# Kernel tuning notes

Hardware: AMD Instinct MI355X
Metric: run time of the kernel (lower is better)

Reference implementation:

```python
import jax, jax.numpy as jnp
import numpy as np

B = 512          # graphs
NODES = 90       # nodes per graph (fixed by lin1 = Linear(90*L*H, ...))
N = B * NODES    # total nodes
F_IN = 90        # dataset.num_features
H = 128          # hidden
L = 3            # num_layers
HL = 64          # hidden_linear
C = 2            # dataset.num_classes
DEG = 16         # avg degree
E = N * DEG      # total edges


def setup_inputs() -> dict:
    key = jax.random.key(0)
    ks = jax.random.split(key, 14)
    x = jax.random.normal(ks[0], (N, F_IN), jnp.float32)
    # intra-graph random edges: graph g owns nodes [g*90, (g+1)*90)
    g = jnp.repeat(jnp.arange(B), NODES * DEG)
    src = g * NODES + jax.random.randint(ks[1], (E,), 0, NODES)
    dst = g * NODES + jax.random.randint(ks[2], (E,), 0, NODES)
    edge_index = jnp.stack([src, dst]).astype(jnp.int64)
    edge_attr = jax.random.uniform(ks[3], (E,), jnp.float32, 0.1, 1.0)
    batch = jnp.repeat(jnp.arange(B), NODES).astype(jnp.int64)

    def lin(k, fi, fo):
        s = 1.0 / np.sqrt(fi)
        kw, kb = jax.random.split(k)
        return (jax.random.uniform(kw, (fi, fo), jnp.float32, -s, s),
                jax.random.uniform(kb, (fo,), jnp.float32, -s, s))

    W1, b1 = lin(ks[4], F_IN, H)
    W2, b2 = lin(ks[5], H, H)
    W3, b3 = lin(ks[6], H, H)
    lin1_W, lin1_b = lin(ks[7], NODES * L * H, HL)
    lin2_W, lin2_b = lin(ks[8], HL, C)
    return {"x": x, "edge_attr": edge_attr, "W1": W1, "b1": b1, "W2": W2,
            "b2": b2, "W3": W3, "b3": b3, "lin1_W": lin1_W, "lin1_b": lin1_b,
            "lin2_W": lin2_W, "lin2_b": lin2_b, "edge_index": edge_index,
            "batch": batch}


def reference(x, edge_attr, W1, b1, W2, b2, W3, b3, lin1_W, lin1_b,
              lin2_W, lin2_b, edge_index, batch):
    src, dst = edge_index[0], edge_index[1]
    # GCN normalization with added self-loops (weight 1), as in PyG GCNConv
    loop = jnp.arange(N)
    s = jnp.concatenate([src, loop])
    d = jnp.concatenate([dst, loop])
    w = jnp.concatenate([edge_attr, jnp.ones((N,), x.dtype)])
    deg = jax.ops.segment_sum(w, d, num_segments=N)
    dis = jnp.where(deg > 0, jax.lax.rsqrt(jnp.maximum(deg, 1e-30)), 0.0)
    norm = dis[s] * w * dis[d]  # [E+N]

    def conv(h, W, b):
        h = h @ W                                  # [N, H]
        msg = norm[:, None] * h[s]                 # gather+scale [E+N, H]
        return jax.ops.segment_sum(msg, d, num_segments=N) + b

    h1 = jax.nn.relu(conv(x, W1, b1))
    h2 = jax.nn.relu(conv(h1, W2, b2))
    h3 = jax.nn.relu(conv(h2, W3, b3))
    xc = jnp.concatenate([h1, h2, h3], axis=1)     # [N, L*H]
    # to_dense_batch: every graph has exactly 90 nodes in order, so no padding
    # (fill_value never appears) and dense batching is a pure reshape.
    z = xc.reshape(B, NODES * L * H)
    h = jax.nn.relu(z @ lin1_W + lin1_b)
    logits = h @ lin2_W + lin2_b                   # dropout is identity in eval
    return jax.nn.log_softmax(logits, axis=-1)
```

## Files before the change

### kernel.cpp

```cpp
#include <hip/hip_runtime.h>

typedef __bf16 bfx8 __attribute__((ext_vector_type(8)));
typedef float fx4 __attribute__((ext_vector_type(4)));
typedef unsigned short us4 __attribute__((ext_vector_type(4)));
typedef unsigned short us8 __attribute__((ext_vector_type(8)));

#define NNODES 90
#define NPAD   96
#define HF     128
#define NGRAPH 512
#define EPG    1440
#define ETOT   (NGRAPH*EPG)
#define KTOT   34560
#define NKTOT  1080
#define KSPLIT 45
#define KSTEPS (NKTOT/KSPLIT)

__device__ __forceinline__ unsigned short f2bf(float f){
  union { float f; unsigned u; } v; v.f = f;
  return (unsigned short)((v.u + 0x7FFFu + ((v.u>>16)&1u)) >> 16);
}
__device__ __forceinline__ int hsw(int node, int f){
  return node*HF + ((((f>>3) ^ (node&15)))<<3) + (f&7);
}

__global__ __launch_bounds__(256) void pack_all_kern(
    const float* __restrict__ W1,
    const float* __restrict__ W2,
    const float* __restrict__ W3,
    const float* __restrict__ L1W,
    unsigned short* __restrict__ o1,
    unsigned short* __restrict__ o2,
    unsigned short* __restrict__ o3,
    unsigned short* __restrict__ l1p,
    float* __restrict__ accf)
{
  __shared__ __align__(16) unsigned short tile[32*64];
  int b = blockIdx.x;
  int t = threadIdx.x;
  if (b < NKTOT) {
    int ks = b;
#pragma unroll
    for (int j=0;j<8;j++) tile[t*8+j] = f2bf(L1W[ks*32*64 + t*8 + j]);
    __syncthreads();
    int lane = t & 63;
    int nt = t >> 6;
    int n  = nt*16 + (lane&15);
    int kq = (lane>>4)*8;
    us8 v;
#pragma unroll
    for (int j=0;j<8;j++) v[j] = tile[(kq+j)*64 + n];
    *(us8*)&l1p[((nt*NKTOT + ks)*64 + lane)*8] = v;
  } else if (b < NKTOT + 22) {
    int bb = b - NKTOT;
    const float* W; unsigned short* out; int K, nK, tt;
    if (bb < 6)       { W = W1; out = o1; K = 90;  nK = 3; tt = bb*256 + t; }
    else if (bb < 14) { W = W2; out = o2; K = 128; nK = 4; tt = (bb-6)*256 + t; }
    else              { W = W3; out = o3; K = 128; nK = 4; tt = (bb-14)*256 + t; }
    int lane = tt & 63;
    int ks = (tt>>6) % nK;
    int nt = (tt>>6) / nK;
    int n  = nt*16 + (lane&15);
    int k0 = ks*32 + (lane>>4)*8;
    unsigned short v[8];
#pragma unroll
    for (int j=0;j<8;j++){ int k=k0+j; v[j] = (k<K)? f2bf(W[k*128+n]) : (unsigned short)0; }
    unsigned short* o = out + ((nt*nK+ks)*64 + lane)*8;
#pragma unroll
    for (int j=0;j<8;j++) o[j]=v[j];
  } else {
    int base = (b - (NKTOT+22))*16384 + t*4;
#pragma unroll
    for (int i = 0; i < 16; ++i) {
      fx4 z = {0.f,0.f,0.f,0.f};
      *(fx4*)&accf[base + i*1024] = z;
    }
  }
}

__global__ __launch_bounds__(512) void gcn_layers_kern(
    const float* __restrict__ x,
    const float* __restrict__ eattr,
    const int* __restrict__ ei,
    const unsigned short* __restrict__ w1p,
    const unsigned short* __restrict__ w2p,
    const unsigned short* __restrict__ w3p,
    const float* __restrict__ b1,
    const float* __restrict__ b2,
    const float* __restrict__ b3,
    unsigned short* __restrict__ xc)
{
  __shared__ __align__(16) char smem[65280];
  unsigned short* Abf = (unsigned short*)smem;
  unsigned short* H   = (unsigned short*)(smem + 17280);
  unsigned short* Tt  = (unsigned short*)(smem + 40320);
  float* Af  = (float*)(smem + 17280);
  float* deg = (float*)(smem + 64896);

  const int g = blockIdx.x;
  const int tid = threadIdx.x;
  const int lane = tid & 63, wave = tid >> 6;
  const int q = lane >> 4, r = lane & 15;
  const int eb = g*EPG;
  const int nb = g*NNODES;
  const long long* e64 = (const long long*)ei;

  bool i64f;
  {
    int v = ei[2*lane + 1];
    i64f = (__ballot(v != 0) == 0ull);
  }

  const int e0 = tid, e1 = tid + 512, e2 = tid + 1024;
  const bool h2 = (e2 < EPG);
  int s0, d0, s1, d1, s2 = nb, d2 = nb;
  if (i64f) {
    s0 = (int)e64[eb+e0]; d0 = (int)e64[ETOT+eb+e0];
    s1 = (int)e64[eb+e1]; d1 = (int)e64[ETOT+eb+e1];
    if (h2) { s2 = (int)e64[eb+e2]; d2 = (int)e64[ETOT+eb+e2]; }
  } else {
    s0 = ei[eb+e0]; d0 = ei[ETOT+eb+e0];
    s1 = ei[eb+e1]; d1 = ei[ETOT+eb+e1];
    if (h2) { s2 = ei[eb+e2]; d2 = ei[ETOT+eb+e2]; }
  }
  float w0 = eattr[eb+e0];
  float w1 = eattr[eb+e1];
  float w2 = h2 ? eattr[eb+e2] : 0.f;

  for (int i = tid*4; i < NNODES*NPAD; i += 512*4) {
    fx4 zv = {0.f,0.f,0.f,0.f};
    *(fx4*)&Af[i] = zv;
  }
  __syncthreads();
  atomicAdd(&Af[(d0-nb)*NPAD + (s0-nb)], w0);
  atomicAdd(&Af[(d1-nb)*NPAD + (s1-nb)], w1);
  if (h2) atomicAdd(&Af[(d2-nb)*NPAD + (s2-nb)], w2);
  __syncthreads();
  {
    int l16 = tid & 15;
    for (int row = tid >> 4; row < NPAD; row += 32) {
      float s = 0.f;
      if (row < NNODES) {
#pragma unroll
        for (int j = 0; j < 6; ++j) s += Af[row*NPAD + l16 + 16*j];
      }
      s += __shfl_xor(s, 1);
      s += __shfl_xor(s, 2);
      s += __shfl_xor(s, 4);
      s += __shfl_xor(s, 8);
      if (l16 == 0) deg[row] = (row < NNODES) ? rsqrtf(1.f + s) : 1.0f;
    }
  }
  __syncthreads();
  for (int i = tid; i < NNODES*NPAD; i += 512) {
    int row = i / NPAD, col = i - row*NPAD;
    float a = Af[i];
    if (col == row) a += 1.0f;
    Abf[i] = f2bf(a * deg[row] * deg[col]);
  }
  __syncthreads();
  for (int i = tid; i < NNODES*90; i += 512) {
    int node = i/90, f = i - node*90;
    H[hsw(node, f)] = f2bf(x[(nb + node)*90 + f]);
  }
  for (int i = tid; i < NNODES*6; i += 512) {
    int node = i/6, f = 90 + (i - node*6);
    H[hsw(node, f)] = 0;
  }
  __syncthreads();

#pragma unroll
  for (int l = 0; l < 3; ++l) {
    const unsigned short* wpk = (l==0)? w1p : (l==1)? w2p : w3p;
    const float* bias         = (l==0)? b1 : (l==1)? b2 : b3;
    const int nK = (l==0)? 3 : 4;

    bfx8 wf[4];
#pragma unroll
    for (int ks = 0; ks < 4; ++ks)
      if (ks < nK) wf[ks] = *(const bfx8*)(const void*)&wpk[((wave*nK + ks)*64 + lane)*8];

    for (int mt = 0; mt < 6; ++mt) {
      int row = mt*16 + r; if (row > 89) row = 89;
      fx4 acc = {0.f,0.f,0.f,0.f};
#pragma unroll
      for (int ks = 0; ks < 4; ++ks)
        if (ks < nK) {
          bfx8 af = *(const bfx8*)(const void*)&H[row*HF + (((4*ks + q) ^ (row&15))<<3)];
          acc = __builtin_amdgcn_mfma_f32_16x16x32_bf16(af, wf[ks], acc, 0,0,0);
        }
      us4 o;
#pragma unroll
      for (int i2=0;i2<4;i2++) o[i2] = f2bf(acc[i2]);
      *(us4*)&Tt[(wave*16 + r)*NPAD + mt*16 + q*4] = o;
    }
    __syncthreads();

    {
      bfx8 tf[3];
#pragma unroll
      for (int ks = 0; ks < 3; ++ks)
        tf[ks] = *(const bfx8*)(const void*)&Tt[(wave*16 + r)*NPAD + ks*32 + q*8];
      float bv[4];
#pragma unroll
      for (int i2=0;i2<4;i2++) bv[i2] = bias[wave*16 + q*4 + i2];
      for (int nt = 0; nt < 6; ++nt) {
        int arow = nt*16 + r; if (arow > 89) arow = 89;
        fx4 acc = {0.f,0.f,0.f,0.f};
#pragma unroll
        for (int ks = 0; ks < 3; ++ks) {
          bfx8 bfr = *(const bfx8*)(const void*)&Abf[arow*NPAD + ks*32 + q*8];
          acc = __builtin_amdgcn_mfma_f32_16x16x32_bf16(tf[ks], bfr, acc, 0,0,0);
        }
        int m = nt*16 + r;
        if (m < NNODES) {
          us4 o;
#pragma unroll
          for (int i2=0;i2<4;i2++){
            float v = acc[i2] + bv[i2];
            o[i2] = f2bf(v > 0.f ? v : 0.f);
          }
          *(us4*)&H[m*HF + (((2*wave + (q>>1)) ^ (m&15))<<3) + (q&1)*4] = o;
        }
      }
    }
    __syncthreads();

    for (int i = tid*8; i < NNODES*HF; i += 512*8) {
      int node = i >> 7, p = (i >> 3) & 15;
      us8 v = *(const us8*)&H[i];
      int f0 = (p ^ (node&15)) << 3;
      *(us8*)&xc[(nb + node)*384 + l*128 + f0] = v;
    }
  }
}

__global__ __launch_bounds__(256) void gemm2_kern(
    const unsigned short* __restrict__ z,
    const unsigned short* __restrict__ wp,
    float* __restrict__ accf)
{
  int mb = blockIdx.x % 16;
  int kb = blockIdx.x / 16;
  int tid = threadIdx.x;
  int lane = tid & 63, wave = tid >> 6;
  int q = lane >> 4, r = lane & 15;
  int mt = wave >> 1;
  int nt0 = (wave & 1)*2;
  int m0 = mb*32;

  const unsigned short* zbase = &z[(m0 + mt*16 + r)*KTOT + (kb*KSTEPS)*32 + q*8];
  const unsigned short* wb0   = &wp[((nt0+0)*NKTOT + kb*KSTEPS)*512 + lane*8];
  const unsigned short* wb1   = &wp[((nt0+1)*NKTOT + kb*KSTEPS)*512 + lane*8];

  fx4 acc0 = {0,0,0,0}, acc1 = {0,0,0,0};
#pragma unroll 4
  for (int it = 0; it < KSTEPS; ++it) {
    bfx8 af = *(const bfx8*)(const void*)&zbase[it*32];
    bfx8 bA = *(const bfx8*)(const void*)&wb0[it*512];
    bfx8 bB = *(const bfx8*)(const void*)&wb1[it*512];
    acc0 = __builtin_amdgcn_mfma_f32_16x16x32_bf16(af, bA, acc0, 0,0,0);
    acc1 = __builtin_amdgcn_mfma_f32_16x16x32_bf16(af, bB, acc1, 0,0,0);
  }
#pragma unroll
  for (int i2 = 0; i2 < 4; ++i2) {
    int row = m0 + mt*16 + q*4 + i2;
    atomicAdd(&accf[row*64 + (nt0+0)*16 + r], acc0[i2]);
    atomicAdd(&accf[row*64 + (nt0+1)*16 + r], acc1[i2]);
  }
}

__global__ __launch_bounds__(256) void head_kern(
    const float* __restrict__ accf,
    const float* __restrict__ l1b,
    const float* __restrict__ l2w,
    const float* __restrict__ l2b,
    float* __restrict__ out)
{
  int gph = blockIdx.x*4 + (threadIdx.x >> 6);
  int j = threadIdx.x & 63;
  float h = accf[gph*64 + j] + l1b[j];
  h = h > 0.f ? h : 0.f;
  float p0 = h * l2w[2*j];
  float p1 = h * l2w[2*j+1];
  for (int off = 32; off; off >>= 1) {
    p0 += __shfl_down(p0, off);
    p1 += __shfl_down(p1, off);
  }
  if (j == 0) {
    float l0 = p0 + l2b[0];
    float l1 = p1 + l2b[1];
    float mx = fmaxf(l0, l1);
    float lse = mx + logf(expf(l0-mx) + expf(l1-mx));
    out[gph*2]   = l0 - lse;
    out[gph*2+1] = l1 - lse;
  }
}

extern "C" void kernel_launch(void* const* d_in, const int* in_sizes, int n_in,
                              void* d_out, int out_size, void* d_ws, size_t ws_size,
                              hipStream_t stream)
{
  const float* x   = (const float*)d_in[0];
  const float* ea  = (const float*)d_in[1];
  const float* W1  = (const float*)d_in[2];
  const float* b1  = (const float*)d_in[3];
  const float* W2  = (const float*)d_in[4];
  const float* b2  = (const float*)d_in[5];
  const float* W3  = (const float*)d_in[6];
  const float* b3  = (const float*)d_in[7];
  const float* L1W = (const float*)d_in[8];
  const float* L1b = (const float*)d_in[9];
  const float* L2W = (const float*)d_in[10];
  const float* L2b = (const float*)d_in[11];
  const int* ei    = (const int*)d_in[12];
  float* out       = (float*)d_out;

  char* ws = (char*)d_ws;
  unsigned short* xc  = (unsigned short*)(ws);
  unsigned short* l1p = (unsigned short*)(ws + 35389440);
  unsigned short* w1p = (unsigned short*)(ws + 39813120);
  unsigned short* w2p = (unsigned short*)(ws + 39837696);
  unsigned short* w3p = (unsigned short*)(ws + 39870464);
  float* accf         = (float*)(ws + 39903232);

  pack_all_kern<<<NKTOT + 22 + 2, 256, 0, stream>>>(W1, W2, W3, L1W,
                                                    w1p, w2p, w3p, l1p, accf);
  gcn_layers_kern<<<NGRAPH, 512, 0, stream>>>(x, ea, ei, w1p, w2p, w3p,
                                              b1, b2, b3, xc);
  gemm2_kern<<<16*KSPLIT, 256, 0, stream>>>(xc, l1p, accf);
  head_kern<<<NGRAPH/4, 256, 0, stream>>>(accf, L1b, L2W, L2b, out);
}
```

Measured before the change: 144.4 us.

## Replace atomic split-K reduction with partial buffers summed in head kernel

The lin1 GEMM now gives each wave a 16-row tile across all 64 output columns, so every A-fragment load feeds four MFMAs instead of two. Blocks cover 64 rows, halving the block count. Each split-K slice writes its partial sums to its own slot in a buffer rather than atomically adding into a zeroed accumulator. The zeroing pass in the pack kernel is removed, and the head kernel sums the 45 partial slices itself. The cost is a larger partial buffer (45×512×64 floats) and a serial 45-step reduction per output in the head kernel.

After: 145.2 us. About the same (+0.6%).

```diff
diff --git a/kernel.cpp b/kernel.cpp
--- a/kernel.cpp
+++ b/kernel.cpp
@@ -32,8 +32,7 @@
     unsigned short* __restrict__ o1,
     unsigned short* __restrict__ o2,
     unsigned short* __restrict__ o3,
-    unsigned short* __restrict__ l1p,
-    float* __restrict__ accf)
+    unsigned short* __restrict__ l1p)
 {
   __shared__ __align__(16) unsigned short tile[32*64];
   int b = blockIdx.x;
@@ -51,7 +50,7 @@
 #pragma unroll
     for (int j=0;j<8;j++) v[j] = tile[(kq+j)*64 + n];
     *(us8*)&l1p[((nt*NKTOT + ks)*64 + lane)*8] = v;
-  } else if (b < NKTOT + 22) {
+  } else {
     int bb = b - NKTOT;
     const float* W; unsigned short* out; int K, nK, tt;
     if (bb < 6)       { W = W1; out = o1; K = 90;  nK = 3; tt = bb*256 + t; }
@@ -68,13 +67,6 @@
     unsigned short* o = out + ((nt*nK+ks)*64 + lane)*8;
 #pragma unroll
     for (int j=0;j<8;j++) o[j]=v[j];
-  } else {
-    int base = (b - (NKTOT+22))*16384 + t*4;
-#pragma unroll
-    for (int i = 0; i < 16; ++i) {
-      fx4 z = {0.f,0.f,0.f,0.f};
-      *(fx4*)&accf[base + i*1024] = z;
-    }
   }
 }
 
@@ -238,40 +230,38 @@
 __global__ __launch_bounds__(256) void gemm2_kern(
     const unsigned short* __restrict__ z,
     const unsigned short* __restrict__ wp,
-    float* __restrict__ accf)
-{
-  int mb = blockIdx.x % 16;
-  int kb = blockIdx.x / 16;
+    float* __restrict__ pbuf)
+{
+  int mb = blockIdx.x % 8;
+  int kb = blockIdx.x / 8;
   int tid = threadIdx.x;
   int lane = tid & 63, wave = tid >> 6;
   int q = lane >> 4, r = lane & 15;
-  int mt = wave >> 1;
-  int nt0 = (wave & 1)*2;
-  int m0 = mb*32;
-
-  const unsigned short* zbase = &z[(m0 + mt*16 + r)*KTOT + (kb*KSTEPS)*32 + q*8];
-  const unsigned short* wb0   = &wp[((nt0+0)*NKTOT + kb*KSTEPS)*512 + lane*8];
-  const unsigned short* wb1   = &wp[((nt0+1)*NKTOT + kb*KSTEPS)*512 + lane*8];
-
-  fx4 acc0 = {0,0,0,0}, acc1 = {0,0,0,0};
+  int m0 = mb*64;
+
+  const unsigned short* zbase = &z[(m0 + wave*16 + r)*KTOT + (kb*KSTEPS)*32 + q*8];
+  const unsigned short* wb = &wp[(kb*KSTEPS)*512 + lane*8];
+
+  fx4 acc[4] = {{0,0,0,0},{0,0,0,0},{0,0,0,0},{0,0,0,0}};
 #pragma unroll 4
   for (int it = 0; it < KSTEPS; ++it) {
     bfx8 af = *(const bfx8*)(const void*)&zbase[it*32];
-    bfx8 bA = *(const bfx8*)(const void*)&wb0[it*512];
-    bfx8 bB = *(const bfx8*)(const void*)&wb1[it*512];
-    acc0 = __builtin_amdgcn_mfma_f32_16x16x32_bf16(af, bA, acc0, 0,0,0);
-    acc1 = __builtin_amdgcn_mfma_f32_16x16x32_bf16(af, bB, acc1, 0,0,0);
-  }
-#pragma unroll
-  for (int i2 = 0; i2 < 4; ++i2) {
-    int row = m0 + mt*16 + q*4 + i2;
-    atomicAdd(&accf[row*64 + (nt0+0)*16 + r], acc0[i2]);
-    atomicAdd(&accf[row*64 + (nt0+1)*16 + r], acc1[i2]);
-  }
+#pragma unroll
+    for (int nt = 0; nt < 4; ++nt) {
+      bfx8 bf = *(const bfx8*)(const void*)&wb[(nt*NKTOT + it)*512];
+      acc[nt] = __builtin_amdgcn_mfma_f32_16x16x32_bf16(af, bf, acc[nt], 0,0,0);
+    }
+  }
+  float* pb = &pbuf[(kb*NGRAPH + m0 + wave*16)*64];
+#pragma unroll
+  for (int nt = 0; nt < 4; ++nt)
+#pragma unroll
+    for (int i2 = 0; i2 < 4; ++i2)
+      pb[(q*4 + i2)*64 + nt*16 + r] = acc[nt][i2];
 }
 
 __global__ __launch_bounds__(256) void head_kern(
-    const float* __restrict__ accf,
+    const float* __restrict__ pbuf,
     const float* __restrict__ l1b,
     const float* __restrict__ l2w,
     const float* __restrict__ l2b,
@@ -279,7 +269,9 @@
 {
   int gph = blockIdx.x*4 + (threadIdx.x >> 6);
   int j = threadIdx.x & 63;
-  float h = accf[gph*64 + j] + l1b[j];
+  float h = l1b[j];
+  for (int kb = 0; kb < KSPLIT; ++kb)
+    h += pbuf[(kb*NGRAPH + gph)*64 + j];
   h = h > 0.f ? h : 0.f;
   float p0 = h * l2w[2*j];
   float p1 = h * l2w[2*j+1];
@@ -322,12 +314,12 @@
   unsigned short* w1p = (unsigned short*)(ws + 39813120);
   unsigned short* w2p = (unsigned short*)(ws + 39837696);
   unsigned short* w3p = (unsigned short*)(ws + 39870464);
-  float* accf         = (float*)(ws + 39903232);
-
-  pack_all_kern<<<NKTOT + 22 + 2, 256, 0, stream>>>(W1, W2, W3, L1W,
-                                                    w1p, w2p, w3p, l1p, accf);
+  float* pbuf         = (float*)(ws + 39903232);
+
+  pack_all_kern<<<NKTOT + 22, 256, 0, stream>>>(W1, W2, W3, L1W,
+                                                w1p, w2p, w3p, l1p);
   gcn_layers_kern<<<NGRAPH, 512, 0, stream>>>(x, ea, ei, w1p, w2p, w3p,
                                               b1, b2, b3, xc);
-  gemm2_kern<<<16*KSPLIT, 256, 0, stream>>>(xc, l1p, accf);
-  head_kern<<<NGRAPH/4, 256, 0, stream>>>(accf, L1b, L2W, L2b, out);
-}
+  gemm2_kern<<<8*KSPLIT, 256, 0, stream>>>(xc, l1p, pbuf);
+  head_kern<<<NGRAPH/4, 256, 0, stream>>>(pbuf, L1b, L2W, L2b, out);
+}
```
